# Optimization experiments

Measured on AMD Instinct MI355X. Metric: run time of the kernel, lower is better.

Reference implementation:

```python
import jax, jax.numpy as jnp
import numpy as np

N, K = 524288, 128

def setup_inputs() -> dict:
    key = jax.random.key(0)
    k1, k2 = jax.random.split(key)
    inputs = jax.random.normal(k1, (N, K), dtype=jnp.float32)
    target = jax.random.uniform(k2, (N, K), dtype=jnp.float32)
    return {"input": inputs, "target": target}

def reference(input, target):
    # Equivalent to: for each class y, cum += target[:, y] * cross_entropy(input, y)
    # cross_entropy(input, y) = -log_softmax(input)[:, y], so the loop reduces to a
    # single log_softmax and a weighted row-sum against the target probabilities.
    log_p = jax.nn.log_softmax(input, axis=-1)          # [n, k]
    cum_losses = -jnp.sum(target * log_p, axis=-1)       # [n]
    return jnp.mean(cum_losses)                          # reduction='mean'
```

## Files before the change

kernel.cpp:

```cpp
#include <hip/hip_runtime.h>
#include <math.h>


#define KDIM 128
#define BLOCK 256
#define GRID 2048
#define UNROLL 4

typedef float v4f __attribute__((ext_vector_type(4)));

__global__ __launch_bounds__(BLOCK, 8) void sce_partial_kernel(
    const float* __restrict__ x, const float* __restrict__ t,
    float* __restrict__ partials, int n_rows) {
    const int tid  = threadIdx.x;
    const int lane = tid & 63;
    const int wave_in_block = tid >> 6;
    const int wave_id = blockIdx.x * (BLOCK / 64) + wave_in_block;
    const int n_waves = GRID * (BLOCK / 64);
    const int n_pairs = n_rows >> 1;

    float acc = 0.0f;

    int p0 = wave_id * UNROLL;
    unsigned off = (unsigned)p0 * (2 * KDIM) + (unsigned)lane * 4;
    const unsigned stride_elems = (unsigned)n_waves * UNROLL * (2 * KDIM);
    const int pair_stride = n_waves * UNROLL;

    for (; p0 + UNROLL <= n_pairs; p0 += pair_stride, off += stride_elems) {
        v4f xv[UNROLL], tv[UNROLL];
        #pragma unroll
        for (int u = 0; u < UNROLL; ++u) {
            xv[u] = __builtin_nontemporal_load(
                        reinterpret_cast<const v4f*>(x + off + u * (2 * KDIM)));
            tv[u] = __builtin_nontemporal_load(
                        reinterpret_cast<const v4f*>(t + off + u * (2 * KDIM)));
        }

        float e[UNROLL];
        #pragma unroll
        for (int u = 0; u < UNROLL; ++u)
            e[u] = (__expf(xv[u].x) + __expf(xv[u].y)) +
                   (__expf(xv[u].z) + __expf(xv[u].w));

        #pragma unroll
        for (int o = 16; o >= 1; o >>= 1) {
            #pragma unroll
            for (int u = 0; u < UNROLL; ++u)
                e[u] += __shfl_xor(e[u], o, 64);
        }

        #pragma unroll
        for (int u = 0; u < UNROLL; ++u) {
            const float ts = (tv[u].x + tv[u].y) + (tv[u].z + tv[u].w);
            float dt = tv[u].x * xv[u].x;
            dt = fmaf(tv[u].y, xv[u].y, dt);
            dt = fmaf(tv[u].z, xv[u].z, dt);
            dt = fmaf(tv[u].w, xv[u].w, dt);
            acc += fmaf(ts, __logf(e[u]), -dt);
        }
    }

    for (; p0 < n_pairs; ++p0, off += 2 * KDIM) {
        const v4f xv = __builtin_nontemporal_load(
                           reinterpret_cast<const v4f*>(x + off));
        const v4f tv = __builtin_nontemporal_load(
                           reinterpret_cast<const v4f*>(t + off));
        float e = (__expf(xv.x) + __expf(xv.y)) + (__expf(xv.z) + __expf(xv.w));
        #pragma unroll
        for (int o = 16; o >= 1; o >>= 1)
            e += __shfl_xor(e, o, 64);
        const float ts = (tv.x + tv.y) + (tv.z + tv.w);
        const float dt = tv.x * xv.x + tv.y * xv.y + tv.z * xv.z + tv.w * xv.w;
        acc += ts * __logf(e) - dt;
    }

    #pragma unroll
    for (int o = 32; o >= 1; o >>= 1)
        acc += __shfl_xor(acc, o, 64);

    __shared__ float ws[BLOCK / 64];
    if (lane == 0) ws[wave_in_block] = acc;
    __syncthreads();
    if (tid == 0) {
        float s = 0.0f;
        #pragma unroll
        for (int i = 0; i < BLOCK / 64; ++i) s += ws[i];
        partials[blockIdx.x] = s;
    }
}

__global__ __launch_bounds__(256) void sce_finalize_kernel(
    const float* __restrict__ partials, float* __restrict__ out,
    int n_partials, float inv_n) {
    float s = 0.0f;
    for (int i = threadIdx.x; i < n_partials; i += 256) s += partials[i];
    #pragma unroll
    for (int o = 32; o >= 1; o >>= 1) s += __shfl_xor(s, o, 64);
    __shared__ float ws[4];
    const int lane = threadIdx.x & 63, w = threadIdx.x >> 6;
    if (lane == 0) ws[w] = s;
    __syncthreads();
    if (threadIdx.x == 0) {
        float tot = 0.0f;
        #pragma unroll
        for (int i = 0; i < 4; ++i) tot += ws[i];
        out[0] = tot * inv_n;
    }
}

extern "C" void kernel_launch(void* const* d_in, const int* in_sizes, int n_in,
                              void* d_out, int out_size, void* d_ws, size_t ws_size,
                              hipStream_t stream) {
    const float* x = (const float*)d_in[0];
    const float* t = (const float*)d_in[1];
    float* out = (float*)d_out;
    float* partials = (float*)d_ws;

    const int n_rows = in_sizes[0] / KDIM;

    sce_partial_kernel<<<GRID, BLOCK, 0, stream>>>(x, t, partials, n_rows);
    sce_finalize_kernel<<<1, 256, 0, stream>>>(partials, out, GRID,
                                               1.0f / (float)n_rows);
}
```

Before: 470.5 us.

## Software-pipeline row-pair loads with double-buffered registers in grid-stride loop

After: 468.6 us. Within noise of the previous version (-0.4%).

```diff
diff --git a/kernel.cpp b/kernel.cpp
--- a/kernel.cpp
+++ b/kernel.cpp
@@ -5,9 +5,13 @@
 #define KDIM 128
 #define BLOCK 256
 #define GRID 2048
-#define UNROLL 4
+#define UB 2
 
 typedef float v4f __attribute__((ext_vector_type(4)));
+
+__device__ __forceinline__ v4f ntload(const float* p) {
+    return __builtin_nontemporal_load(reinterpret_cast<const v4f*>(p));
+}
 
 __global__ __launch_bounds__(BLOCK, 8) void sce_partial_kernel(
     const float* __restrict__ x, const float* __restrict__ t,
@@ -21,62 +25,108 @@
 
     float acc = 0.0f;
 
-    int p0 = wave_id * UNROLL;
+    const int p0      = wave_id * UB;
+    const int pstride = n_waves * UB;
     unsigned off = (unsigned)p0 * (2 * KDIM) + (unsigned)lane * 4;
-    const unsigned stride_elems = (unsigned)n_waves * UNROLL * (2 * KDIM);
-    const int pair_stride = n_waves * UNROLL;
+    const unsigned ostride = (unsigned)pstride * (2 * KDIM);
 
-    for (; p0 + UNROLL <= n_pairs; p0 += pair_stride, off += stride_elems) {
-        v4f xv[UNROLL], tv[UNROLL];
+    int nb = 0;
+    if (p0 + UB <= n_pairs) nb = (n_pairs - UB - p0) / pstride + 1;
+
+    v4f xa0, ta0, xa1, ta1, xb0, tb0, xb1, tb1;
+    float e0, e1, ts0, ts1;
+
+    auto loadb = [&](v4f& X0, v4f& T0, v4f& X1, v4f& T1, unsigned o) {
+        X0 = ntload(x + o);
+        T0 = ntload(t + o);
+        X1 = ntload(x + o + 2 * KDIM);
+        T1 = ntload(t + o + 2 * KDIM);
+    };
+
+    auto consume = [&](const v4f& X0, const v4f& T0,
+                       const v4f& X1, const v4f& T1) {
+        e0 = (__expf(X0.x) + __expf(X0.y)) + (__expf(X0.z) + __expf(X0.w));
+        ts0 = (T0.x + T0.y) + (T0.z + T0.w);
+        float dt_ = T0.x * X0.x;
+        dt_ = fmaf(T0.y, X0.y, dt_);
+        dt_ = fmaf(T0.z, X0.z, dt_);
+        dt_ = fmaf(T0.w, X0.w, dt_);
+        acc -= dt_;
+        e1 = (__expf(X1.x) + __expf(X1.y)) + (__expf(X1.z) + __expf(X1.w));
+        ts1 = (T1.x + T1.y) + (T1.z + T1.w);
+        float du_ = T1.x * X1.x;
+        du_ = fmaf(T1.y, X1.y, du_);
+        du_ = fmaf(T1.z, X1.z, du_);
+        du_ = fmaf(T1.w, X1.w, du_);
+        acc -= du_;
+    };
+
+    auto finish = [&]() {
         #pragma unroll
-        for (int u = 0; u < UNROLL; ++u) {
-            xv[u] = __builtin_nontemporal_load(
-                        reinterpret_cast<const v4f*>(x + off + u * (2 * KDIM)));
-            tv[u] = __builtin_nontemporal_load(
-                        reinterpret_cast<const v4f*>(t + off + u * (2 * KDIM)));
+        for (int o_ = 16; o_ >= 1; o_ >>= 1) {
+            e0 += __shfl_xor(e0, o_, 64);
+            e1 += __shfl_xor(e1, o_, 64);
         }
+        acc = fmaf(ts0, __logf(e0), acc);
+        acc = fmaf(ts1, __logf(e1), acc);
+    };
 
-        float e[UNROLL];
-        #pragma unroll
-        for (int u = 0; u < UNROLL; ++u)
-            e[u] = (__expf(xv[u].x) + __expf(xv[u].y)) +
-                   (__expf(xv[u].z) + __expf(xv[u].w));
+    if (nb > 0) {
+        loadb(xa0, ta0, xa1, ta1, off);
+        off += ostride;
+        consume(xa0, ta0, xa1, ta1);
+        int b = 1;
+        #pragma unroll 1
+        for (; b + 1 < nb; b += 2) {
+            loadb(xb0, tb0, xb1, tb1, off);
+            off += ostride;
+            finish();
+            consume(xb0, tb0, xb1, tb1);
+            loadb(xa0, ta0, xa1, ta1, off);
+            off += ostride;
+            finish();
+            consume(xa0, ta0, xa1, ta1);
+        }
+        if (b < nb) {
+            loadb(xb0, tb0, xb1, tb1, off);
+            off += ostride;
+            finish();
+            consume(xb0, tb0, xb1, tb1);
+        }
+        finish();
+    }
 
-        #pragma unroll
-        for (int o = 16; o >= 1; o >>= 1) {
+    if (wave_id == 0) {
+        const int mm = n_pairs % pstride;
+        for (int p = n_pairs - (mm % UB); p < n_pairs; ++p) {
+            const unsigned o = (unsigned)p * (2 * KDIM) + (unsigned)lane * 4;
+            const v4f xv = ntload(x + o);
+            const v4f tv = ntload(t + o);
+            float e = (__expf(xv.x) + __expf(xv.y)) + (__expf(xv.z) + __expf(xv.w));
             #pragma unroll
-            for (int u = 0; u < UNROLL; ++u)
-                e[u] += __shfl_xor(e[u], o, 64);
+            for (int o_ = 16; o_ >= 1; o_ >>= 1) e += __shfl_xor(e, o_, 64);
+            const float ts = (tv.x + tv.y) + (tv.z + tv.w);
+            const float dt = tv.x * xv.x + tv.y * xv.y + tv.z * xv.z + tv.w * xv.w;
+            acc += ts * __logf(e) - dt;
         }
-
-        #pragma unroll
-        for (int u = 0; u < UNROLL; ++u) {
-            const float ts = (tv[u].x + tv[u].y) + (tv[u].z + tv[u].w);
-            float dt = tv[u].x * xv[u].x;
-            dt = fmaf(tv[u].y, xv[u].y, dt);
-            dt = fmaf(tv[u].z, xv[u].z, dt);
-            dt = fmaf(tv[u].w, xv[u].w, dt);
-            acc += fmaf(ts, __logf(e[u]), -dt);
+        if (n_rows & 1) {
+            if (lane < 32) {
+                const unsigned o = (unsigned)(n_rows - 1) * KDIM + (unsigned)lane * 4;
+                const v4f xv = ntload(x + o);
+                const v4f tv = ntload(t + o);
+                float e = (__expf(xv.x) + __expf(xv.y)) + (__expf(xv.z) + __expf(xv.w));
+                #pragma unroll
+                for (int o_ = 16; o_ >= 1; o_ >>= 1) e += __shfl_xor(e, o_, 64);
+                const float ts = (tv.x + tv.y) + (tv.z + tv.w);
+                const float dt = tv.x * xv.x + tv.y * xv.y + tv.z * xv.z + tv.w * xv.w;
+                acc += ts * __logf(e) - dt;
+            }
         }
     }
 
-    for (; p0 < n_pairs; ++p0, off += 2 * KDIM) {
-        const v4f xv = __builtin_nontemporal_load(
-                           reinterpret_cast<const v4f*>(x + off));
-        const v4f tv = __builtin_nontemporal_load(
-                           reinterpret_cast<const v4f*>(t + off));
-        float e = (__expf(xv.x) + __expf(xv.y)) + (__expf(xv.z) + __expf(xv.w));
-        #pragma unroll
-        for (int o = 16; o >= 1; o >>= 1)
-            e += __shfl_xor(e, o, 64);
-        const float ts = (tv.x + tv.y) + (tv.z + tv.w);
-        const float dt = tv.x * xv.x + tv.y * xv.y + tv.z * xv.z + tv.w * xv.w;
-        acc += ts * __logf(e) - dt;
-    }
-
     #pragma unroll
-    for (int o = 32; o >= 1; o >>= 1)
-        acc += __shfl_xor(acc, o, 64);
+    for (int o_ = 32; o_ >= 1; o_ >>= 1)
+        acc += __shfl_xor(acc, o_, 64);
 
     __shared__ float ws[BLOCK / 64];
     if (lane == 0) ws[wave_in_block] = acc;
@@ -95,7 +145,7 @@
     float s = 0.0f;
     for (int i = threadIdx.x; i < n_partials; i += 256) s += partials[i];
     #pragma unroll
-    for (int o = 32; o >= 1; o >>= 1) s += __shfl_xor(s, o, 64);
+    for (int o_ = 32; o_ >= 1; o_ >>= 1) s += __shfl_xor(s, o_, 64);
     __shared__ float ws[4];
     const int lane = threadIdx.x & 63, w = threadIdx.x >> 6;
     if (lane == 0) ws[w] = s;
```
